# Performance work log

Hardware: AMD Instinct MI355X
Metric: run time of the kernel (lower is better)

## Reference

```python
import jax, jax.numpy as jnp
import numpy as np

N_AGENTS = 8
N_ENEMIES = 8
N_ALLIES = 7
H = 64            # rnn_hidden_dim (must be 64: Encoder latent dim hardcoded to 64, fed to fc3)
HEADS = 2         # hpn_head_num
OUT_NORMAL = 6    # output_normal_actions
N_ACTIONS = OUT_NORMAL + N_ENEMIES  # 14, required by expand_as in original code
E_DIM = 8
A_DIM = 8
OWN_DIM = 30
HYPER = 64        # hpn_hyper_dim
ENC_HID = 128     # predict_net_dim
BS = 2048


def _gru_cell(x, h, Wih, Whh, bih, bhh):
    # torch GRUCell math, gate order (r, z, n)
    gi = x @ Wih + bih
    gh = h @ Whh + bhh
    ir, iz, inn = jnp.split(gi, 3, axis=-1)
    hr, hz, hn = jnp.split(gh, 3, axis=-1)
    r = jax.nn.sigmoid(ir + hr)
    z = jax.nn.sigmoid(iz + hz)
    n = jnp.tanh(inn + r * hn)
    return (1.0 - z) * n + z * h


def setup_inputs() -> dict:
    key = jax.random.key(0)
    ks = jax.random.split(key, 48)
    B = BS * N_AGENTS

    def w(k, shape):
        return jax.random.normal(k, shape, dtype=jnp.float32) * 0.05

    he_out = ((E_DIM + 1) * H + 1) * HEADS   # 1154
    ha_out = A_DIM * H * HEADS               # 1024 (non-MMM map)

    return {
        "bs": BS,
        "own_feats": jax.random.normal(ks[0], (B, OWN_DIM), jnp.float32),
        "enemy_feats": jax.random.normal(ks[1], (B * N_ENEMIES, E_DIM), jnp.float32),
        "ally_feats": jax.random.normal(ks[2], (B * N_ALLIES, A_DIM), jnp.float32),
        "agent_ids": jax.random.randint(ks[3], (B,), 0, N_AGENTS),
        "last_action_ids": jax.random.randint(ks[4], (B,), 0, N_ACTIONS),
        "hidden_state": jax.random.normal(ks[5], (B, H), jnp.float32) * 0.1,
        "fc1_own_W": w(ks[6], (OWN_DIM, H)), "fc1_own_b": w(ks[7], (H,)),
        "agent_emb": w(ks[8], (N_AGENTS, H)),
        "action_emb": w(ks[9], (N_ACTIONS, H)),
        "he_W1": w(ks[10], (E_DIM, HYPER)), "he_b1": w(ks[11], (HYPER,)),
        "he_W2": w(ks[12], (HYPER, he_out)), "he_b2": w(ks[13], (he_out,)),
        "ha_W1": w(ks[14], (A_DIM, HYPER)), "ha_b1": w(ks[15], (HYPER,)),
        "ha_W2": w(ks[16], (HYPER, ha_out)), "ha_b2": w(ks[17], (ha_out,)),
        "merger_in_w": jnp.ones((1, HEADS, H), jnp.float32),
        "merger_out_w": jnp.ones((1, HEADS, 1), jnp.float32),
        "gru_Wih": w(ks[18], (H, 3 * H)), "gru_Whh": w(ks[19], (H, 3 * H)),
        "gru_bih": w(ks[20], (3 * H,)), "gru_bhh": w(ks[21], (3 * H,)),
        "fc2n_W": w(ks[22], (H, OUT_NORMAL)), "fc2n_b": w(ks[23], (OUT_NORMAL,)),
        "fc1b_W": w(ks[24], (OWN_DIM, H)), "fc1b_b": w(ks[25], (H,)),
        "gru2_Wih": w(ks[26], (H, 3 * H)), "gru2_Whh": w(ks[27], (H, 3 * H)),
        "gru2_bih": w(ks[28], (3 * H,)), "gru2_bhh": w(ks[29], (3 * H,)),
        "enc_W1": w(ks[30], (H, ENC_HID)), "enc_b1": w(ks[31], (ENC_HID,)),
        "enc_W2": w(ks[32], (ENC_HID, H)), "enc_b2": w(ks[33], (H,)),
        "fc3_W": w(ks[34], (H, N_ACTIONS)), "fc3_b": w(ks[35], (N_ACTIONS,)),
        "mlp_W": w(ks[36], (N_AGENTS, H, N_ACTIONS)), "mlp_b": w(ks[37], (N_AGENTS, N_ACTIONS)),
    }


def reference(bs, own_feats, enemy_feats, ally_feats, agent_ids, last_action_ids,
              hidden_state, fc1_own_W, fc1_own_b, agent_emb, action_emb,
              he_W1, he_b1, he_W2, he_b2, ha_W1, ha_b1, ha_W2, ha_b2,
              merger_in_w, merger_out_w, gru_Wih, gru_Whh, gru_bih, gru_bhh,
              fc2n_W, fc2n_b, fc1b_W, fc1b_b, gru2_Wih, gru2_Whh, gru2_bih, gru2_bhh,
              enc_W1, enc_b1, enc_W2, enc_b2, fc3_W, fc3_b, mlp_W, mlp_b):
    B = bs * N_AGENTS

    # own embedding + id/action embeddings
    emb_own = own_feats @ fc1_own_W + fc1_own_b
    emb_own = emb_own + agent_emb[agent_ids] + action_emb[last_action_ids]

    # hypernet-generated per-enemy fc1 weights, applied per entity, summed over enemies
    he = jax.nn.relu(enemy_feats @ he_W1 + he_b1) @ he_W2 + he_b2  # [B*E, 1154]
    cut = (H + 1) * HEADS
    w1e = he[:, :-cut].reshape(-1, E_DIM, H * HEADS)               # [B*E, e_dim, H*heads]
    emb_en = jnp.einsum('nd,ndk->nk', enemy_feats, w1e)
    emb_en = emb_en.reshape(B, N_ENEMIES, HEADS, H).sum(axis=1)    # [B, heads, H]

    ha = jax.nn.relu(ally_feats @ ha_W1 + ha_b1) @ ha_W2 + ha_b2   # [B*A, 1024]
    w1a = ha.reshape(-1, A_DIM, H * HEADS)
    emb_al = jnp.einsum('nd,ndk->nk', ally_feats, w1a)
    emb_al = emb_al.reshape(B, N_ALLIES, HEADS, H).sum(axis=1)     # [B, heads, H]

    # Merger over heads (softmax-weighted sum)
    mw = jax.nn.softmax(merger_in_w, axis=1)                       # [1, heads, H]
    merged = jnp.sum(mw * (emb_en + emb_al), axis=1)               # [B, H]

    x = jax.nn.relu(emb_own + merged)
    hh = _gru_cell(x, hidden_state, gru_Wih, gru_Whh, gru_bih, gru_bhh)  # [B, H]

    q_normal = (hh @ fc2n_W + fc2n_b).reshape(bs, N_AGENTS, OUT_NORMAL)

    # hypernet-generated attack output heads
    w2 = he[:, -cut:-HEADS].reshape(B, N_ENEMIES, H, HEADS)
    w2 = w2.transpose(0, 2, 1, 3).reshape(B, H, N_ENEMIES * HEADS)
    b2 = he[:, -HEADS:].reshape(B, N_ENEMIES * HEADS)
    qa = jnp.einsum('bh,bhk->bk', hh, w2) + b2                     # [B, E*heads]
    qa = qa.reshape(B * N_ENEMIES, HEADS)
    mo = jax.nn.softmax(merger_out_w[:, :, 0], axis=1)             # [1, heads]
    q_attack = jnp.sum(mo * qa, axis=1).reshape(bs, N_AGENTS, N_ENEMIES)

    q = jnp.concatenate([q_normal, q_attack], axis=-1)             # [bs, n_agents, 14]

    # parallel fc1 -> single-step GRU -> encoder branch
    x2 = jax.nn.relu(own_feats @ fc1b_W + fc1b_b)                  # [B, H]
    g = _gru_cell(x2, hidden_state, gru2_Wih, gru2_Whh, gru2_bih, gru2_bhh)  # [B, H]
    z = jax.nn.relu(g @ enc_W1 + enc_b1) @ enc_W2 + enc_b2         # [B, 64] encoder latent
    q_f = (z @ fc3_W + fc3_b).reshape(bs, N_AGENTS, N_ACTIONS)

    # per-agent mlps applied to first n_agents rows of gru output (as in original)
    ga = g[:N_AGENTS]                                              # [n_agents, H]
    local_q = jnp.einsum('ah,ahk->ak', ga, mlp_W) + mlp_b          # [n_agents, n_actions]
    local_qe = jnp.broadcast_to(local_q[None], q.shape)

    q_total = q + local_qe + q_f
    return (q_total, hh.reshape(bs, N_AGENTS, H), local_qe, q_f)
```

## Files before the change

### kernel.cpp

```cpp
#include <hip/hip_runtime.h>

#define HH_OFF 229376
#define LQE_OFF 1277952
#define QF_OFF 1507328

#define WS_HE 0
#define WS_HA 33280
#define WS_ATT 66560
#define WS_BATT 70656
#define WS_BH 70720
#define WS_BC 70784
#define WS_LQ 70800
#define WS_G1 70912
#define WS_G2 95488
#define WS_E1 120064
#define WS_E2 128256
#define WS_F1 136448
#define WS_END 140544

#define SSTR 648

struct Params {
  const float *own, *ef, *af, *hid;
  const int *aid, *lid;
  const float *fc1oW, *fc1ob, *aemb, *actemb;
  const float *heW1, *heb1, *heW2, *heb2;
  const float *haW1, *hab1, *haW2, *hab2;
  const float *mi, *mo;
  const float *gWih, *gWhh, *gbih, *gbhh;
  const float *fc2nW, *fc2nb;
  const float *fc1bW, *fc1bb;
  const float *g2Wih, *g2Whh, *g2bih, *g2bhh;
  const float *eW1, *eb1, *eW2, *eb2;
  const float *fc3W, *fc3b;
  const float *mlpW, *mlpb;
};

__device__ __forceinline__ float sigm(float x) {
  x = fminf(fmaxf(x, -30.f), 30.f);
  return 1.f / (1.f + __expf(-x));
}
__device__ __forceinline__ float tanh_(float x) {
  x = fminf(fmaxf(x, -15.f), 15.f);
  float e = __expf(-2.f * x);
  return (1.f - e) / (1.f + e);
}

__global__ void __launch_bounds__(512) prep_kernel(Params p, float* __restrict__ ws) {
  const int tid = threadIdx.x;
  if (blockIdx.x == 0) {
    __shared__ float g8[8][64];
    __shared__ float x2s[8][64];
    const int w = __builtin_amdgcn_readfirstlane(tid >> 6);
    const int lane = tid & 63;
    {
      float acc = p.fc1bb[lane];
      const float* ow = p.own + w * 30;
      for (int d = 0; d < 30; ++d) acc += ow[d] * p.fc1bW[d * 64 + lane];
      x2s[w][lane] = fmaxf(acc, 0.f);
      float a0 = p.g2bih[lane], a1 = p.g2bih[64 + lane], a2 = p.g2bih[128 + lane];
      float b0 = p.g2bhh[lane], b1 = p.g2bhh[64 + lane], b2 = p.g2bhh[128 + lane];
      const float* hidw = p.hid + w * 64;
      for (int k = 0; k < 64; ++k) {
        float xk = x2s[w][k];
        float hk = hidw[k];
        a0 += xk * p.g2Wih[k * 192 + lane];
        a1 += xk * p.g2Wih[k * 192 + 64 + lane];
        a2 += xk * p.g2Wih[k * 192 + 128 + lane];
        b0 += hk * p.g2Whh[k * 192 + lane];
        b1 += hk * p.g2Whh[k * 192 + 64 + lane];
        b2 += hk * p.g2Whh[k * 192 + 128 + lane];
      }
      float r = sigm(a0 + b0), z = sigm(a1 + b1);
      float n = tanh_(a2 + r * b2);
      g8[w][lane] = (1.f - z) * n + z * hidw[lane];
    }
    __syncthreads();
    if (tid < 112) {
      int a = tid / 14, c = tid % 14;
      float lacc = p.mlpb[a * 14 + c];
      for (int h = 0; h < 64; ++h) lacc += g8[a][h] * p.mlpW[(a * 64 + h) * 14 + c];
      ws[WS_LQ + tid] = lacc;
    }
    return;
  }
  const int idx = (int)(blockIdx.x - 1) * 512 + tid;
  if (idx >= WS_END) return;
  const float mo0 = sigm(p.mo[0] - p.mo[1]);
  const float mo1 = 1.f - mo0;
  if (idx < 33280) {
    int c = idx >> 8, rem = idx & 255, h = rem >> 2, q = rem & 3;
    int t = c * 4 + q;
    float mw0 = sigm(p.mi[h] - p.mi[64 + h]);
    float mw1 = 1.f - mw0;
    float v;
    if (t < 512) {
      int d = t >> 6, j = t & 63;
      v = mw0 * p.heW2[j * 1154 + d * 128 + h] + mw1 * p.heW2[j * 1154 + d * 128 + 64 + h];
    } else {
      int d = t - 512;
      v = mw0 * p.heb2[d * 128 + h] + mw1 * p.heb2[d * 128 + 64 + h];
    }
    ws[WS_HE + idx] = v;
  } else if (idx < 66560) {
    int rel = idx - 33280;
    int c = rel >> 8, rem = rel & 255, h = rem >> 2, q = rem & 3;
    int t = c * 4 + q;
    float mw0 = sigm(p.mi[h] - p.mi[64 + h]);
    float mw1 = 1.f - mw0;
    float v;
    if (t < 512) {
      int d = t >> 6, j = t & 63;
      v = mw0 * p.haW2[j * 1024 + d * 128 + h] + mw1 * p.haW2[j * 1024 + d * 128 + 64 + h];
    } else {
      int d = t - 512;
      v = mw0 * p.hab2[d * 128 + h] + mw1 * p.hab2[d * 128 + 64 + h];
    }
    ws[WS_HA + rel] = v;
  } else if (idx < 70656) {
    int rel = idx - 66560;
    int c = rel >> 8, rem = rel & 255, j = rem >> 2, q = rem & 3;
    int h = c * 4 + q;
    ws[WS_ATT + rel] = mo0 * p.heW2[j * 1154 + 1024 + 2 * h] +
                       mo1 * p.heW2[j * 1154 + 1024 + 2 * h + 1];
  } else if (idx < 70720) {
    int j = idx - 70656;
    ws[WS_BATT + j] = mo0 * p.heW2[j * 1154 + 1152] + mo1 * p.heW2[j * 1154 + 1153];
  } else if (idx < 70784) {
    int h = idx - 70720;
    ws[WS_BH + h] = mo0 * p.heb2[1024 + 2 * h] + mo1 * p.heb2[1024 + 2 * h + 1];
  } else if (idx == 70784) {
    ws[WS_BC] = mo0 * p.heb2[1152] + mo1 * p.heb2[1153];
  } else if (idx < WS_G1) {
    return;
  } else if (idx < WS_G2) {
    int rel = idx - WS_G1;
    int k4 = rel / 1536, r2 = rel % 1536;
    int j = r2 >> 8, lane = (r2 & 255) >> 2, q = rel & 3;
    int row = 4 * k4 + q;
    ws[idx] = (j < 3) ? p.gWih[row * 192 + j * 64 + lane]
                      : p.gWhh[row * 192 + (j - 3) * 64 + lane];
  } else if (idx < WS_E1) {
    int rel = idx - WS_G2;
    int k4 = rel / 1536, r2 = rel % 1536;
    int j = r2 >> 8, lane = (r2 & 255) >> 2, q = rel & 3;
    int row = 4 * k4 + q;
    ws[idx] = (j < 3) ? p.g2Wih[row * 192 + j * 64 + lane]
                      : p.g2Whh[row * 192 + (j - 3) * 64 + lane];
  } else if (idx < WS_E2) {
    int rel = idx - WS_E1;
    int k4 = rel >> 9, j = (rel >> 8) & 1, lane = (rel & 255) >> 2, q = rel & 3;
    int row = 4 * k4 + q;
    ws[idx] = p.eW1[row * 128 + j * 64 + lane];
  } else if (idx < WS_F1) {
    int rel = idx - WS_E2;
    int k4 = rel >> 8, lane = (rel & 255) >> 2, q = rel & 3;
    int row = 4 * k4 + q;
    ws[idx] = p.eW2[row * 64 + lane];
  } else {
    int rel = idx - WS_F1;
    int k4 = rel >> 9, j = (rel >> 8) & 1, lane = (rel & 255) >> 2, q = rel & 3;
    int row = 4 * k4 + q;
    float v;
    if (row < 30) v = (j == 0) ? p.fc1oW[row * 64 + lane] : p.fc1bW[row * 64 + lane];
    else if (row == 30) v = (j == 0) ? p.fc1ob[lane] : p.fc1bb[lane];
    else v = 0.f;
    ws[idx] = v;
  }
}

__global__ void __launch_bounds__(256, 3) main_kernel(Params p, const float* __restrict__ ws,
                                                      float* __restrict__ out) {
  __shared__ float smem[4 * 4 * SSTR];
  const int w = __builtin_amdgcn_readfirstlane((int)(threadIdx.x >> 6));
  const int lane = threadIdx.x & 63;
  float* S = &smem[w * 4 * SSTR];
  const int i0 = blockIdx.x * 16 + w * 4;

#pragma unroll
  for (int s = 0; s < 4; ++s) {
    S[s * SSTR + 520 + lane] = p.ef[(i0 + s) * 64 + lane];
    if (lane < 56) S[s * SSTR + 584 + lane] = p.af[(i0 + s) * 56 + lane];
  }
  float macc[4] = {0.f, 0.f, 0.f, 0.f};
  {
    float w1[8];
#pragma unroll
    for (int d = 0; d < 8; ++d) w1[d] = p.heW1[d * 64 + lane];
    const float b1 = p.heb1[lane];
#pragma unroll
    for (int s = 0; s < 4; ++s) {
      float T[8], fs[8];
#pragma unroll
      for (int d = 0; d < 8; ++d) { T[d] = 0.f; fs[d] = 0.f; }
#pragma unroll
      for (int e = 0; e < 8; ++e) {
        float4 a = *(const float4*)&S[s * SSTR + 520 + e * 8];
        float4 b = *(const float4*)&S[s * SSTR + 520 + e * 8 + 4];
        float acc = b1 + a.x * w1[0] + a.y * w1[1] + a.z * w1[2] + a.w * w1[3] +
                    b.x * w1[4] + b.y * w1[5] + b.z * w1[6] + b.w * w1[7];
        float r = fmaxf(acc, 0.f);
        T[0] += r * a.x; T[1] += r * a.y; T[2] += r * a.z; T[3] += r * a.w;
        T[4] += r * b.x; T[5] += r * b.y; T[6] += r * b.z; T[7] += r * b.w;
        fs[0] += a.x; fs[1] += a.y; fs[2] += a.z; fs[3] += a.w;
        fs[4] += b.x; fs[5] += b.y; fs[6] += b.z; fs[7] += b.w;
      }
#pragma unroll
      for (int d = 0; d < 8; ++d) S[s * SSTR + d * 64 + lane] = T[d];
      if (lane == 0) {
#pragma unroll
        for (int d = 0; d < 8; ++d) S[s * SSTR + 512 + d] = fs[d];
      }
    }
  }
  {
    const float4* W4 = (const float4*)(ws + WS_HE);
    for (int c = 0; c < 130; ++c) {
      float4 wv = W4[c * 64 + lane];
#pragma unroll
      for (int s = 0; s < 4; ++s) {
        float4 tv = *(const float4*)&S[s * SSTR + c * 4];
        macc[s] += tv.x * wv.x + tv.y * wv.y + tv.z * wv.z + tv.w * wv.w;
      }
    }
  }
  {
    float w1[8];
#pragma unroll
    for (int d = 0; d < 8; ++d) w1[d] = p.haW1[d * 64 + lane];
    const float b1 = p.hab1[lane];
#pragma unroll
    for (int s = 0; s < 4; ++s) {
      float T[8], fs[8];
#pragma unroll
      for (int d = 0; d < 8; ++d) { T[d] = 0.f; fs[d] = 0.f; }
#pragma unroll
      for (int e = 0; e < 7; ++e) {
        float4 a = *(const float4*)&S[s * SSTR + 584 + e * 8];
        float4 b = *(const float4*)&S[s * SSTR + 584 + e * 8 + 4];
        float acc = b1 + a.x * w1[0] + a.y * w1[1] + a.z * w1[2] + a.w * w1[3] +
                    b.x * w1[4] + b.y * w1[5] + b.z * w1[6] + b.w * w1[7];
        float r = fmaxf(acc, 0.f);
        T[0] += r * a.x; T[1] += r * a.y; T[2] += r * a.z; T[3] += r * a.w;
        T[4] += r * b.x; T[5] += r * b.y; T[6] += r * b.z; T[7] += r * b.w;
        fs[0] += a.x; fs[1] += a.y; fs[2] += a.z; fs[3] += a.w;
        fs[4] += b.x; fs[5] += b.y; fs[6] += b.z; fs[7] += b.w;
      }
#pragma unroll
      for (int d = 0; d < 8; ++d) S[s * SSTR + d * 64 + lane] = T[d];
      if (lane == 0) {
#pragma unroll
        for (int d = 0; d < 8; ++d) S[s * SSTR + 512 + d] = fs[d];
      }
    }
  }
  {
    const float4* W4 = (const float4*)(ws + WS_HA);
    for (int c = 0; c < 130; ++c) {
      float4 wv = W4[c * 64 + lane];
#pragma unroll
      for (int s = 0; s < 4; ++s) {
        float4 tv = *(const float4*)&S[s * SSTR + c * 4];
        macc[s] += tv.x * wv.x + tv.y * wv.y + tv.z * wv.z + tv.w * wv.w;
      }
    }
  }
#pragma unroll
  for (int s = 0; s < 4; ++s) {
    S[s * SSTR + 64 + lane] = p.hid[(i0 + s) * 64 + lane];
    if (lane < 32)
      S[s * SSTR + 584 + lane] =
          (lane < 30) ? p.own[(i0 + s) * 30 + lane] : (lane == 30 ? 1.f : 0.f);
  }
  {
    float aO[4] = {0.f, 0.f, 0.f, 0.f}, aB[4] = {0.f, 0.f, 0.f, 0.f};
    const float4* F = (const float4*)(ws + WS_F1);
    for (int k4 = 0; k4 < 8; ++k4) {
      float4 wo = F[k4 * 128 + lane];
      float4 wb = F[k4 * 128 + 64 + lane];
#pragma unroll
      for (int s = 0; s < 4; ++s) {
        float4 o4 = *(const float4*)&S[s * SSTR + 584 + k4 * 4];
        aO[s] += o4.x * wo.x + o4.y * wo.y + o4.z * wo.z + o4.w * wo.w;
        aB[s] += o4.x * wb.x + o4.y * wb.y + o4.z * wb.z + o4.w * wb.w;
      }
    }
#pragma unroll
    for (int s = 0; s < 4; ++s) {
      const int i = i0 + s;
      float x = aO[s] + p.aemb[p.aid[i] * 64 + lane] + p.actemb[p.lid[i] * 64 + lane] + macc[s];
      S[s * SSTR + lane] = fmaxf(x, 0.f);
      S[s * SSTR + 384 + lane] = fmaxf(aB[s], 0.f);
    }
  }
  {
    const float bi0 = p.gbih[lane] + p.gbhh[lane];
    const float bi1 = p.gbih[64 + lane] + p.gbhh[64 + lane];
    const float bi2i = p.gbih[128 + lane];
    const float bi2h = p.gbhh[128 + lane];
    float A0[4], A1[4], A2[4], B2[4];
#pragma unroll
    for (int s = 0; s < 4; ++s) { A0[s] = bi0; A1[s] = bi1; A2[s] = bi2i; B2[s] = bi2h; }
    const float4* G = (const float4*)(ws + WS_G1);
    for (int k4 = 0; k4 < 16; ++k4) {
      float4 w0 = G[k4 * 384 + lane];
      float4 w1v = G[k4 * 384 + 64 + lane];
      float4 w2v = G[k4 * 384 + 128 + lane];
      float4 w3 = G[k4 * 384 + 192 + lane];
      float4 w4v = G[k4 * 384 + 256 + lane];
      float4 w5 = G[k4 * 384 + 320 + lane];
#pragma unroll
      for (int s = 0; s < 4; ++s) {
        float4 x4 = *(const float4*)&S[s * SSTR + k4 * 4];
        float4 h4 = *(const float4*)&S[s * SSTR + 64 + k4 * 4];
        A0[s] += x4.x * w0.x + x4.y * w0.y + x4.z * w0.z + x4.w * w0.w +
                 h4.x * w3.x + h4.y * w3.y + h4.z * w3.z + h4.w * w3.w;
        A1[s] += x4.x * w1v.x + x4.y * w1v.y + x4.z * w1v.z + x4.w * w1v.w +
                 h4.x * w4v.x + h4.y * w4v.y + h4.z * w4v.z + h4.w * w4v.w;
        A2[s] += x4.x * w2v.x + x4.y * w2v.y + x4.z * w2v.z + x4.w * w2v.w;
        B2[s] += h4.x * w5.x + h4.y * w5.y + h4.z * w5.z + h4.w * w5.w;
      }
    }
#pragma unroll
    for (int s = 0; s < 4; ++s) {
      float r = sigm(A0[s]);
      float z = sigm(A1[s]);
      float n = tanh_(A2[s] + r * B2[s]);
      float hp = S[s * SSTR + 64 + lane];
      float hh = (1.f - z) * n + z * hp;
      S[s * SSTR + 128 + lane] = hh;
      out[HH_OFF + (i0 + s) * 64 + lane] = hh;
    }
  }
  const int so = lane / 14, co = lane % 14;
  float qn = 0.f;
  if (lane < 56 && co < 6) {
    float acc = p.fc2nb[co];
    for (int h = 0; h < 64; ++h) acc += S[so * SSTR + 128 + h] * p.fc2nW[h * 6 + co];
    qn = acc;
  }
  {
    float v4[4];
    const float batt = ws[WS_BATT + lane];
#pragma unroll
    for (int s = 0; s < 4; ++s) v4[s] = batt;
    const float4* A4 = (const float4*)(ws + WS_ATT);
    for (int c = 0; c < 16; ++c) {
      float4 wv = A4[c * 64 + lane];
#pragma unroll
      for (int s = 0; s < 4; ++s) {
        float4 h4 = *(const float4*)&S[s * SSTR + 128 + c * 4];
        v4[s] += h4.x * wv.x + h4.y * wv.y + h4.z * wv.z + h4.w * wv.w;
      }
    }
    float w1[8];
#pragma unroll
    for (int d = 0; d < 8; ++d) w1[d] = p.heW1[d * 64 + lane];
    const float b1 = p.heb1[lane];
    const float bhv = ws[WS_BH + lane];
    const float bc = ws[WS_BC];
#pragma unroll
    for (int s = 0; s < 4; ++s) {
      float red[9];
#pragma unroll
      for (int e = 0; e < 8; ++e) {
        float4 a = *(const float4*)&S[s * SSTR + 520 + e * 8];
        float4 b = *(const float4*)&S[s * SSTR + 520 + e * 8 + 4];
        float acc = b1 + a.x * w1[0] + a.y * w1[1] + a.z * w1[2] + a.w * w1[3] +
                    b.x * w1[4] + b.y * w1[5] + b.z * w1[6] + b.w * w1[7];
        red[e] = fmaxf(acc, 0.f) * v4[s];
      }
      red[8] = S[s * SSTR + 128 + lane] * bhv;
#pragma unroll
      for (int off = 32; off >= 1; off >>= 1) {
#pragma unroll
        for (int t = 0; t < 9; ++t) red[t] += __shfl_xor(red[t], off, 64);
      }
      if (lane == 0) {
#pragma unroll
        for (int e = 0; e < 8; ++e) S[s * SSTR + 448 + 6 + e] = red[e] + red[8] + bc;
      }
    }
  }
  {
    const float bi0 = p.g2bih[lane] + p.g2bhh[lane];
    const float bi1 = p.g2bih[64 + lane] + p.g2bhh[64 + lane];
    const float bi2i = p.g2bih[128 + lane];
    const float bi2h = p.g2bhh[128 + lane];
    float A0[4], A1[4], A2[4], B2[4];
#pragma unroll
    for (int s = 0; s < 4; ++s) { A0[s] = bi0; A1[s] = bi1; A2[s] = bi2i; B2[s] = bi2h; }
    const float4* G = (const float4*)(ws + WS_G2);
    for (int k4 = 0; k4 < 16; ++k4) {
      float4 w0 = G[k4 * 384 + lane];
      float4 w1v = G[k4 * 384 + 64 + lane];
      float4 w2v = G[k4 * 384 + 128 + lane];
      float4 w3 = G[k4 * 384 + 192 + lane];
      float4 w4v = G[k4 * 384 + 256 + lane];
      float4 w5 = G[k4 * 384 + 320 + lane];
#pragma unroll
      for (int s = 0; s < 4; ++s) {
        float4 x4 = *(const float4*)&S[s * SSTR + 384 + k4 * 4];
        float4 h4 = *(const float4*)&S[s * SSTR + 64 + k4 * 4];
        A0[s] += x4.x * w0.x + x4.y * w0.y + x4.z * w0.z + x4.w * w0.w +
                 h4.x * w3.x + h4.y * w3.y + h4.z * w3.z + h4.w * w3.w;
        A1[s] += x4.x * w1v.x + x4.y * w1v.y + x4.z * w1v.z + x4.w * w1v.w +
                 h4.x * w4v.x + h4.y * w4v.y + h4.z * w4v.z + h4.w * w4v.w;
        A2[s] += x4.x * w2v.x + x4.y * w2v.y + x4.z * w2v.z + x4.w * w2v.w;
        B2[s] += h4.x * w5.x + h4.y * w5.y + h4.z * w5.z + h4.w * w5.w;
      }
    }
#pragma unroll
    for (int s = 0; s < 4; ++s) {
      float r = sigm(A0[s]);
      float z = sigm(A1[s]);
      float n = tanh_(A2[s] + r * B2[s]);
      float hp = S[s * SSTR + 64 + lane];
      S[s * SSTR + 192 + lane] = (1.f - z) * n + z * hp;
    }
  }
  {
    float C0[4], C1[4];
#pragma unroll
    for (int s = 0; s < 4; ++s) { C0[s] = p.eb1[lane]; C1[s] = p.eb1[64 + lane]; }
    const float4* E1 = (const float4*)(ws + WS_E1);
    for (int k4 = 0; k4 < 16; ++k4) {
      float4 w0 = E1[k4 * 128 + lane];
      float4 w1v = E1[k4 * 128 + 64 + lane];
#pragma unroll
      for (int s = 0; s < 4; ++s) {
        float4 g4 = *(const float4*)&S[s * SSTR + 192 + k4 * 4];
        C0[s] += g4.x * w0.x + g4.y * w0.y + g4.z * w0.z + g4.w * w0.w;
        C1[s] += g4.x * w1v.x + g4.y * w1v.y + g4.z * w1v.z + g4.w * w1v.w;
      }
    }
#pragma unroll
    for (int s = 0; s < 4; ++s) {
      S[s * SSTR + 256 + lane] = fmaxf(C0[s], 0.f);
      S[s * SSTR + 320 + lane] = fmaxf(C1[s], 0.f);
    }
  }
  {
    float Z[4];
#pragma unroll
    for (int s = 0; s < 4; ++s) Z[s] = p.eb2[lane];
    const float4* E2 = (const float4*)(ws + WS_E2);
    for (int k4 = 0; k4 < 32; ++k4) {
      float4 wv = E2[k4 * 64 + lane];
#pragma unroll
      for (int s = 0; s < 4; ++s) {
        float4 z4 = *(const float4*)&S[s * SSTR + 256 + k4 * 4];
        Z[s] += z4.x * wv.x + z4.y * wv.y + z4.z * wv.z + z4.w * wv.w;
      }
    }
#pragma unroll
    for (int s = 0; s < 4; ++s) S[s * SSTR + 384 + lane] = Z[s];
  }
  if (lane < 56) {
    const int s = so, c = co;
    const int i = i0 + s;
    float qf = p.fc3b[c];
    for (int k = 0; k < 64; ++k) qf += S[s * SSTR + 384 + k] * p.fc3W[k * 14 + c];
    float lq = ws[WS_LQ + (i & 7) * 14 + c];
    float qo = (c < 6) ? qn : S[s * SSTR + 448 + c];
    out[i * 14 + c] = qo + qf + lq;
    out[LQE_OFF + i * 14 + c] = lq;
    out[QF_OFF + i * 14 + c] = qf;
  }
}

extern "C" void kernel_launch(void* const* d_in, const int* in_sizes, int n_in,
                              void* d_out, int out_size, void* d_ws, size_t ws_size,
                              hipStream_t stream) {
  (void)in_sizes; (void)n_in; (void)out_size; (void)ws_size;
  Params p;
  p.own = (const float*)d_in[1];
  p.ef = (const float*)d_in[2];
  p.af = (const float*)d_in[3];
  p.aid = (const int*)d_in[4];
  p.lid = (const int*)d_in[5];
  p.hid = (const float*)d_in[6];
  p.fc1oW = (const float*)d_in[7];
  p.fc1ob = (const float*)d_in[8];
  p.aemb = (const float*)d_in[9];
  p.actemb = (const float*)d_in[10];
  p.heW1 = (const float*)d_in[11];
  p.heb1 = (const float*)d_in[12];
  p.heW2 = (const float*)d_in[13];
  p.heb2 = (const float*)d_in[14];
  p.haW1 = (const float*)d_in[15];
  p.hab1 = (const float*)d_in[16];
  p.haW2 = (const float*)d_in[17];
  p.hab2 = (const float*)d_in[18];
  p.mi = (const float*)d_in[19];
  p.mo = (const float*)d_in[20];
  p.gWih = (const float*)d_in[21];
  p.gWhh = (const float*)d_in[22];
  p.gbih = (const float*)d_in[23];
  p.gbhh = (const float*)d_in[24];
  p.fc2nW = (const float*)d_in[25];
  p.fc2nb = (const float*)d_in[26];
  p.fc1bW = (const float*)d_in[27];
  p.fc1bb = (const float*)d_in[28];
  p.g2Wih = (const float*)d_in[29];
  p.g2Whh = (const float*)d_in[30];
  p.g2bih = (const float*)d_in[31];
  p.g2bhh = (const float*)d_in[32];
  p.eW1 = (const float*)d_in[33];
  p.eb1 = (const float*)d_in[34];
  p.eW2 = (const float*)d_in[35];
  p.eb2 = (const float*)d_in[36];
  p.fc3W = (const float*)d_in[37];
  p.fc3b = (const float*)d_in[38];
  p.mlpW = (const float*)d_in[39];
  p.mlpb = (const float*)d_in[40];
  float* ws = (float*)d_ws;
  float* out = (float*)d_out;
  prep_kernel<<<dim3(276), dim3(512), 0, stream>>>(p, ws);
  main_kernel<<<dim3(1024), dim3(256), 0, stream>>>(p, ws, out);
}
```

Before: 324.4 us.

## Split main kernel into hypernet/GRU kernel and encoder-branch kernel

Splits the single fused kernel into two launches. KernelA runs the hypernetwork, the first GRU and the q outputs. KernelB runs the parallel fc1, the second GRU, the encoder and q_f, and adds q_f into the output written by kernelA. The aim is to cut register and shared-memory pressure per kernel, since kernelB uses a smaller LDS stride. In exchange it adds a kernel launch, re-reads hidden/own inputs, does a read-modify-write on the output, and lowers launch_bounds occupancy hint from 3 to 2.

Result: faster. 309.5 us (-4.6%).

```diff
diff --git a/kernel.cpp b/kernel.cpp
--- a/kernel.cpp
+++ b/kernel.cpp
@@ -19,6 +19,7 @@
 #define WS_END 140544
 
 #define SSTR 648
+#define BSTR 392
 
 struct Params {
   const float *own, *ef, *af, *hid;
@@ -169,8 +170,8 @@
   }
 }
 
-__global__ void __launch_bounds__(256, 3) main_kernel(Params p, const float* __restrict__ ws,
-                                                      float* __restrict__ out) {
+__global__ void __launch_bounds__(256, 2) kernelA(Params p, const float* __restrict__ ws,
+                                                  float* __restrict__ out) {
   __shared__ float smem[4 * 4 * SSTR];
   const int w = __builtin_amdgcn_readfirstlane((int)(threadIdx.x >> 6));
   const int lane = threadIdx.x & 63;
@@ -273,16 +274,14 @@
           (lane < 30) ? p.own[(i0 + s) * 30 + lane] : (lane == 30 ? 1.f : 0.f);
   }
   {
-    float aO[4] = {0.f, 0.f, 0.f, 0.f}, aB[4] = {0.f, 0.f, 0.f, 0.f};
+    float aO[4] = {0.f, 0.f, 0.f, 0.f};
     const float4* F = (const float4*)(ws + WS_F1);
     for (int k4 = 0; k4 < 8; ++k4) {
       float4 wo = F[k4 * 128 + lane];
-      float4 wb = F[k4 * 128 + 64 + lane];
 #pragma unroll
       for (int s = 0; s < 4; ++s) {
         float4 o4 = *(const float4*)&S[s * SSTR + 584 + k4 * 4];
         aO[s] += o4.x * wo.x + o4.y * wo.y + o4.z * wo.z + o4.w * wo.w;
-        aB[s] += o4.x * wb.x + o4.y * wb.y + o4.z * wb.z + o4.w * wb.w;
       }
     }
 #pragma unroll
@@ -290,7 +289,6 @@
       const int i = i0 + s;
       float x = aO[s] + p.aemb[p.aid[i] * 64 + lane] + p.actemb[p.lid[i] * 64 + lane] + macc[s];
       S[s * SSTR + lane] = fmaxf(x, 0.f);
-      S[s * SSTR + 384 + lane] = fmaxf(aB[s], 0.f);
     }
   }
   {
@@ -382,6 +380,45 @@
       }
     }
   }
+  if (lane < 56) {
+    const int s = so, c = co;
+    const int i = i0 + s;
+    float lq = ws[WS_LQ + (i & 7) * 14 + c];
+    float qo = (c < 6) ? qn : S[s * SSTR + 448 + c];
+    out[i * 14 + c] = qo + lq;
+    out[LQE_OFF + i * 14 + c] = lq;
+  }
+}
+
+__global__ void __launch_bounds__(256, 2) kernelB(Params p, const float* __restrict__ ws,
+                                                  float* __restrict__ out) {
+  __shared__ float smem[4 * 4 * BSTR];
+  const int w = __builtin_amdgcn_readfirstlane((int)(threadIdx.x >> 6));
+  const int lane = threadIdx.x & 63;
+  float* S = &smem[w * 4 * BSTR];
+  const int i0 = blockIdx.x * 16 + w * 4;
+
+#pragma unroll
+  for (int s = 0; s < 4; ++s) {
+    S[s * BSTR + 64 + lane] = p.hid[(i0 + s) * 64 + lane];
+    if (lane < 32)
+      S[s * BSTR + 192 + lane] =
+          (lane < 30) ? p.own[(i0 + s) * 30 + lane] : (lane == 30 ? 1.f : 0.f);
+  }
+  {
+    float aB[4] = {0.f, 0.f, 0.f, 0.f};
+    const float4* F = (const float4*)(ws + WS_F1);
+    for (int k4 = 0; k4 < 8; ++k4) {
+      float4 wb = F[k4 * 128 + 64 + lane];
+#pragma unroll
+      for (int s = 0; s < 4; ++s) {
+        float4 o4 = *(const float4*)&S[s * BSTR + 192 + k4 * 4];
+        aB[s] += o4.x * wb.x + o4.y * wb.y + o4.z * wb.z + o4.w * wb.w;
+      }
+    }
+#pragma unroll
+    for (int s = 0; s < 4; ++s) S[s * BSTR + lane] = fmaxf(aB[s], 0.f);
+  }
   {
     const float bi0 = p.g2bih[lane] + p.g2bhh[lane];
     const float bi1 = p.g2bih[64 + lane] + p.g2bhh[64 + lane];
@@ -400,8 +437,8 @@
       float4 w5 = G[k4 * 384 + 320 + lane];
 #pragma unroll
       for (int s = 0; s < 4; ++s) {
-        float4 x4 = *(const float4*)&S[s * SSTR + 384 + k4 * 4];
-        float4 h4 = *(const float4*)&S[s * SSTR + 64 + k4 * 4];
+        float4 x4 = *(const float4*)&S[s * BSTR + k4 * 4];
+        float4 h4 = *(const float4*)&S[s * BSTR + 64 + k4 * 4];
         A0[s] += x4.x * w0.x + x4.y * w0.y + x4.z * w0.z + x4.w * w0.w +
                  h4.x * w3.x + h4.y * w3.y + h4.z * w3.z + h4.w * w3.w;
         A1[s] += x4.x * w1v.x + x4.y * w1v.y + x4.z * w1v.z + x4.w * w1v.w +
@@ -415,8 +452,8 @@
       float r = sigm(A0[s]);
       float z = sigm(A1[s]);
       float n = tanh_(A2[s] + r * B2[s]);
-      float hp = S[s * SSTR + 64 + lane];
-      S[s * SSTR + 192 + lane] = (1.f - z) * n + z * hp;
+      float hp = S[s * BSTR + 64 + lane];
+      S[s * BSTR + 128 + lane] = (1.f - z) * n + z * hp;
     }
   }
   {
@@ -429,15 +466,15 @@
       float4 w1v = E1[k4 * 128 + 64 + lane];
 #pragma unroll
       for (int s = 0; s < 4; ++s) {
-        float4 g4 = *(const float4*)&S[s * SSTR + 192 + k4 * 4];
+        float4 g4 = *(const float4*)&S[s * BSTR + 128 + k4 * 4];
         C0[s] += g4.x * w0.x + g4.y * w0.y + g4.z * w0.z + g4.w * w0.w;
         C1[s] += g4.x * w1v.x + g4.y * w1v.y + g4.z * w1v.z + g4.w * w1v.w;
       }
     }
 #pragma unroll
     for (int s = 0; s < 4; ++s) {
-      S[s * SSTR + 256 + lane] = fmaxf(C0[s], 0.f);
-      S[s * SSTR + 320 + lane] = fmaxf(C1[s], 0.f);
+      S[s * BSTR + 192 + lane] = fmaxf(C0[s], 0.f);
+      S[s * BSTR + 256 + lane] = fmaxf(C1[s], 0.f);
     }
   }
   {
@@ -449,23 +486,20 @@
       float4 wv = E2[k4 * 64 + lane];
 #pragma unroll
       for (int s = 0; s < 4; ++s) {
-        float4 z4 = *(const float4*)&S[s * SSTR + 256 + k4 * 4];
+        float4 z4 = *(const float4*)&S[s * BSTR + 192 + k4 * 4];
         Z[s] += z4.x * wv.x + z4.y * wv.y + z4.z * wv.z + z4.w * wv.w;
       }
     }
 #pragma unroll
-    for (int s = 0; s < 4; ++s) S[s * SSTR + 384 + lane] = Z[s];
+    for (int s = 0; s < 4; ++s) S[s * BSTR + 320 + lane] = Z[s];
   }
   if (lane < 56) {
-    const int s = so, c = co;
+    const int s = lane / 14, c = lane % 14;
     const int i = i0 + s;
     float qf = p.fc3b[c];
-    for (int k = 0; k < 64; ++k) qf += S[s * SSTR + 384 + k] * p.fc3W[k * 14 + c];
-    float lq = ws[WS_LQ + (i & 7) * 14 + c];
-    float qo = (c < 6) ? qn : S[s * SSTR + 448 + c];
-    out[i * 14 + c] = qo + qf + lq;
-    out[LQE_OFF + i * 14 + c] = lq;
+    for (int k = 0; k < 64; ++k) qf += S[s * BSTR + 320 + k] * p.fc3W[k * 14 + c];
     out[QF_OFF + i * 14 + c] = qf;
+    out[i * 14 + c] += qf;
   }
 }
 
@@ -517,5 +551,6 @@
   float* ws = (float*)d_ws;
   float* out = (float*)d_out;
   prep_kernel<<<dim3(276), dim3(512), 0, stream>>>(p, ws);
-  main_kernel<<<dim3(1024), dim3(256), 0, stream>>>(p, ws, out);
+  kernelA<<<dim3(1024), dim3(256), 0, stream>>>(p, ws, out);
+  kernelB<<<dim3(1024), dim3(256), 0, stream>>>(p, ws, out);
 }
```
